# Optimization experiments

Measured on AMD Instinct MI355X. Metric: run time of the kernel, lower is better.

## Reference

```python
import jax, jax.numpy as jnp
import numpy as np

C = 128                  # stem_dim
CONV_DIM = C * C * 3 * 3 # 147456
B, T = 32, 30
N_CH = 1024
N_ANS = 32               # n_answers + 1
V = 44

UNARY = [4,10,11,12,13,14,15,16,17,18,19,20,21,22,23,24,25,29,30,31,32,33,34,35,36,37,38,39,40,41,43]
BINARY = [5,6,7,8,9,26,27,28,42]
SCENE_TOK = 4

_kind = np.zeros(V, np.int32)   # 0=special, 1=scene, 2=unary, 3=binary
_uidx = np.zeros(V, np.int32)
_bidx = np.zeros(V, np.int32)
for _j, _t in enumerate(UNARY):
    _kind[_t] = 2; _uidx[_t] = _j
for _j, _t in enumerate(BINARY):
    _kind[_t] = 3; _bidx[_t] = _j
_kind[SCENE_TOK] = 1
KIND_T, U_T, B_T = jnp.array(_kind), jnp.array(_uidx), jnp.array(_bidx)


def conv3x3(x, w):  # x [N,C,H,W], w [O,I,3,3], pad=1
    return jax.lax.conv_general_dilated(x, w, (1, 1), ((1, 1), (1, 1)),
                                        dimension_numbers=('NCHW', 'OIHW', 'NCHW'))


def conv1x1(x, w):
    return jax.lax.conv_general_dilated(x, w, (1, 1), ((0, 0), (0, 0)),
                                        dimension_numbers=('NCHW', 'OIHW', 'NCHW'))

# per-sample weights: vmap conv over batch
_bconv = jax.vmap(lambda x, w: conv3x3(x[None], w)[0])


def exec_unary(x, w1, w2):
    return jax.nn.relu(_bconv(jax.nn.relu(_bconv(x, w1)), w2))


def exec_binary(x1, x2, w1, w2, w3):
    h = jax.nn.relu(_bconv(jnp.concatenate([x1, x2], axis=1), w1))
    h = jax.nn.relu(_bconv(h, w2))
    return jax.nn.relu(_bconv(h, w3))


def setup_inputs() -> dict:
    key = jax.random.key(0)
    ks = jax.random.split(key, 10)
    std = 1.0 / float(np.sqrt(CONV_DIM))
    r = lambda k, shp, s: jax.random.normal(k, shp, jnp.float32) * s
    return {
        'feats': jax.random.normal(ks[0], (B, N_CH, 14, 14), jnp.float32),
        'programs': jax.random.randint(ks[1], (B, T), 0, V, dtype=jnp.int32),
        'stem_w1': r(ks[2], (C, N_CH, 3, 3), 0.02),
        'stem_b1': jnp.zeros((C,), jnp.float32),
        'stem_w2': r(ks[3], (C, C, 3, 3), 0.05),
        'stem_b2': jnp.zeros((C,), jnp.float32),
        'mem_u': jax.random.uniform(ks[4], (31, 2 * CONV_DIM), jnp.float32, -std, std),
        'mem_b': jax.random.uniform(ks[5], (9, 4 * CONV_DIM), jnp.float32, -std, std),
        'cls_w': r(ks[6], (512, C, 1, 1), 0.05),
        'cls_b': jnp.zeros((512,), jnp.float32),
        'fc1_w': r(ks[7], (1024, 512 * 7 * 7), 0.01),
        'fc1_b': jnp.zeros((1024,), jnp.float32),
        'fc2_w': r(ks[8], (N_ANS, 1024), 0.03),
        'fc2_b': jnp.zeros((N_ANS,), jnp.float32),
    }


def reference(feats, programs, stem_w1, stem_b1, stem_w2, stem_b2, mem_u, mem_b,
              cls_w, cls_b, fc1_w, fc1_b, fc2_w, fc2_b):
    # stem: conv3x3 -> relu -> conv3x3 -> relu
    h = jax.nn.relu(conv3x3(feats, stem_w1) + stem_b1[None, :, None, None])
    feat = jax.nn.relu(conv3x3(h, stem_w2) + stem_b2[None, :, None, None])  # [B,C,14,14]

    def step(carry, tok):  # tok [B] int32
        out, saved = carry
        kind = KIND_T[tok]                           # [B]
        uread = mem_u[U_T[tok]]                      # [B, 2*CONV_DIM] one-hot memory read
        w1 = uread[:, :CONV_DIM].reshape(-1, C, C, 3, 3)
        w2 = uread[:, CONV_DIM:].reshape(-1, C, C, 3, 3)
        bread = mem_b[B_T[tok]]                      # [B, 4*CONV_DIM]
        bw1 = bread[:, :2 * CONV_DIM].reshape(-1, C, 2 * C, 3, 3)
        bw2 = bread[:, 2 * CONV_DIM:3 * CONV_DIM].reshape(-1, C, C, 3, 3)
        bw3 = bread[:, 3 * CONV_DIM:].reshape(-1, C, C, 3, 3)
        is_scene = (kind == 1)[:, None, None, None]
        u_in = jnp.where(is_scene, feat, out)        # scene runs on stem features
        u_out = exec_unary(u_in, w1, w2)
        b_out = exec_binary(out, saved, bw1, bw2, bw3)
        k4 = kind[:, None, None, None]
        new_saved = jnp.where(is_scene, out, saved)  # scene saves current output
        new_out = jnp.where(k4 == 0, out, jnp.where(k4 == 3, b_out, u_out))
        return (new_out, new_saved), None

    toks_rev = programs[:, ::-1].T.astype(jnp.int32)  # [T,B] reversed program
    (out, _), _ = jax.lax.scan(step, (feat, jnp.zeros_like(feat)), toks_rev)

    # classifier: conv1x1 -> relu -> maxpool2 -> flatten -> fc -> relu -> fc
    h = jax.nn.relu(conv1x1(out, cls_w) + cls_b[None, :, None, None])
    h = jax.lax.reduce_window(h, -jnp.inf, jax.lax.max, (1, 1, 2, 2), (1, 1, 2, 2), 'VALID')
    h = h.reshape(h.shape[0], -1)                     # [B, 512*7*7]
    h = jax.nn.relu(h @ fc1_w.T + fc1_b)
    return h @ fc2_w.T + fc2_b                        # [B, N_ANS]
```

## Files before the change

kernel.cpp:

```cpp
#include <hip/hip_runtime.h>


#define NSTEP 30
#define CD 147456
#define P 196
#define FSZ 25088
#define LROW 18
#define LBUF (272*LROW)

typedef __attribute__((ext_vector_type(8))) short short8;
typedef __attribute__((ext_vector_type(16))) float f32x16;

__constant__ int KIND_TBL[44] = {
  0,0,0,0,1,3,3,3,3,3, 2,2,2,2,2,2,2,2,2,2,
  2,2,2,2,2,2,3,3,3,2, 2,2,2,2,2,2,2,2,2,2, 2,2,3,2};
__constant__ int MIDX_TBL[44] = {
  0,0,0,0,0,0,1,2,3,4, 1,2,3,4,5,6,7,8,9,10,
  11,12,13,14,15,16,5,6,7,17, 18,19,20,21,22,23,24,25,26,27, 28,29,8,30};

__device__ __forceinline__ uint32_t bf16_rne(float x) {
  uint32_t u = __float_as_uint(x);
  return (u + 0x7fffu + ((u >> 16) & 1u)) >> 16;
}
__device__ __forceinline__ uint32_t pack_hl(float x) {
  uint32_t h = bf16_rne(x);
  float rest = x - __uint_as_float(h << 16);
  uint32_t l = bf16_rne(rest);
  return (h << 16) | l;
}
__device__ __forceinline__ float ld_sc0(const float* p) {
  return __hip_atomic_load(p, __ATOMIC_RELAXED, __HIP_MEMORY_SCOPE_AGENT);
}

__device__ __forceinline__ void bbar(int* __restrict__ ctr, int target) {
  __syncthreads();
  if (threadIdx.x == 0) {
    __hip_atomic_fetch_add(ctr, 1, __ATOMIC_RELEASE, __HIP_MEMORY_SCOPE_AGENT);
    while (__hip_atomic_load(ctr, __ATOMIC_ACQUIRE, __HIP_MEMORY_SCOPE_AGENT) < target)
      __builtin_amdgcn_s_sleep(2);
  }
  __syncthreads();
}

__global__ void __launch_bounds__(256) repack_kernel(
    const float* __restrict__ sw1, const float* __restrict__ sw2,
    const float* __restrict__ mu, const float* __restrict__ mb,
    uint32_t* __restrict__ Wp)
{
  const int blk = blockIdx.x;
  const int C = blk / 9, tap = blk % 9;
  const float* src; int nic, lc;
  if (C < 64)       { src = sw1; nic = 1024; lc = C; }
  else if (C < 72)  { src = sw2; nic = 128;  lc = C - 64; }
  else if (C < 568) { int u = (C - 72) >> 4, r = (C - 72) & 15;
                      src = mu + (size_t)u * 2 * CD + (size_t)(r >> 3) * CD;
                      nic = 128; lc = r & 7; }
  else              { int j = (C - 568) >> 5, r = (C - 568) & 31;
                      const float* base = mb + (size_t)j * 4 * CD;
                      if (r < 16)      { src = base;                  nic = 256; lc = r; }
                      else if (r < 24) { src = base + 2 * (size_t)CD; nic = 128; lc = r - 16; }
                      else             { src = base + 3 * (size_t)CD; nic = 128; lc = r - 24; } }
  const int mt = threadIdx.x >> 6, lane = threadIdx.x & 63;
  const int oc = mt * 32 + (lane & 31);
  const int ic0 = lc * 16 + (lane >> 5) * 8;
  uint32_t hw[4], lw[4];
#pragma unroll
  for (int pr = 0; pr < 4; ++pr) {
    uint32_t hh[2], ll[2];
#pragma unroll
    for (int e = 0; e < 2; ++e) {
      float x = src[((size_t)oc * nic + (ic0 + pr * 2 + e)) * 9 + tap];
      uint32_t h = bf16_rne(x);
      float rest = x - __uint_as_float(h << 16);
      hh[e] = h; ll[e] = bf16_rne(rest);
    }
    hw[pr] = hh[0] | (hh[1] << 16);
    lw[pr] = ll[0] | (ll[1] << 16);
  }
  uint32_t* dstb = Wp + (size_t)blk * 2048;
  *(uint4*)(dstb + (mt * 2 + 0) * 256 + lane * 4) = make_uint4(hw[0], hw[1], hw[2], hw[3]);
  *(uint4*)(dstb + (mt * 2 + 1) * 256 + lane * 4) = make_uint4(lw[0], lw[1], lw[2], lw[3]);
}

union BU { uint32_t u[4]; uint4 v; short8 s8; };

__device__ __forceinline__ void load_wchunk(const uint32_t* __restrict__ wb,
                                            BU* wh, BU* wl) {
#pragma unroll
  for (int t = 0; t < 9; ++t) {
    wh[t].v = *(const uint4*)(wb + t * 2048);
    wl[t].v = *(const uint4*)(wb + t * 2048 + 256);
  }
}

__device__ __forceinline__ void mfma_chunk(const uint32_t* __restrict__ sb,
                                           int pwbase, const BU* wh, const BU* wl,
                                           f32x16& acc) {
  const int TAPOFF[9] = {0, 1, 2, 16, 17, 18, 32, 33, 34};
#pragma unroll
  for (int tap = 0; tap < 9; ++tap) {
    const int pw = pwbase + TAPOFF[tap] * LROW;
    uint2 q0 = *(const uint2*)(sb + pw);
    uint2 q1 = *(const uint2*)(sb + pw + 2);
    uint2 q2 = *(const uint2*)(sb + pw + 4);
    uint2 q3 = *(const uint2*)(sb + pw + 6);
    BU Bh, Bl;
    Bh.u[0] = __builtin_amdgcn_perm(q0.y, q0.x, 0x07060302u);
    Bh.u[1] = __builtin_amdgcn_perm(q1.y, q1.x, 0x07060302u);
    Bh.u[2] = __builtin_amdgcn_perm(q2.y, q2.x, 0x07060302u);
    Bh.u[3] = __builtin_amdgcn_perm(q3.y, q3.x, 0x07060302u);
    Bl.u[0] = __builtin_amdgcn_perm(q0.y, q0.x, 0x05040100u);
    Bl.u[1] = __builtin_amdgcn_perm(q1.y, q1.x, 0x05040100u);
    Bl.u[2] = __builtin_amdgcn_perm(q2.y, q2.x, 0x05040100u);
    Bl.u[3] = __builtin_amdgcn_perm(q3.y, q3.x, 0x05040100u);
    acc = __builtin_amdgcn_mfma_f32_32x32x16_bf16(wh[tap].s8, Bh.s8, acc, 0, 0, 0);
    acc = __builtin_amdgcn_mfma_f32_32x32x16_bf16(wh[tap].s8, Bl.s8, acc, 0, 0, 0);
    acc = __builtin_amdgcn_mfma_f32_32x32x16_bf16(wl[tap].s8, Bh.s8, acc, 0, 0, 0);
  }
}

__device__ __forceinline__ void conv_run(
    uint32_t sbuf[2][LBUF],
    const float* __restrict__ in0, const float* __restrict__ in1, int split, int nc,
    int C0, int mt,
    const uint32_t* __restrict__ Wp, const float* __restrict__ bias,
    float* __restrict__ dst, float* __restrict__ dst2, float* __restrict__ zb,
    const int* imgoff)
{
  const int tid = threadIdx.x;
  const int w = tid >> 6, lane = tid & 63, l31 = lane & 31, kq = lane >> 5;
  const int ic16 = tid >> 5, pl = tid & 31;
  const int pwbase = (32 * w + l31) * LROW + kq * 8;
  const bool cw = (w < 7);
  const uint32_t* wbase = Wp + (size_t)C0 * 9 * 2048 + (mt * 2) * 256 + lane * 4;

  f32x16 acc;
#pragma unroll
  for (int i = 0; i < 16; ++i) acc[i] = 0.f;

  BU whA[9], wlA[9], whB[9], wlB[9];
  if (cw) load_wchunk(wbase, whA, wlA);
  {
    const float* src = in0 + (size_t)ic16 * P;
#pragma unroll
    for (int i = 0; i < 9; ++i) {
      int p = pl + 32 * i;
      if (p < 272) {
        int off = imgoff[i];
        float x = (off >= 0) ? ld_sc0(src + off) : 0.f;
        sbuf[0][p * LROW + ic16] = pack_hl(x);
      }
    }
  }
  __syncthreads();

  int c = 0;
  while (true) {
    {
      const bool more = c + 1 < nc;
      float sv[9];
      if (more) {
        const int cn = c + 1;
        const float* src = (cn < split) ? in0 + (size_t)(cn * 16 + ic16) * P
                                        : in1 + (size_t)((cn - split) * 16 + ic16) * P;
#pragma unroll
        for (int i = 0; i < 9; ++i) {
          int off = imgoff[i];
          sv[i] = (off >= 0) ? ld_sc0(src + off) : 0.f;
        }
        if (cw) load_wchunk(wbase + (size_t)(c + 1) * 9 * 2048, whB, wlB);
      }
      if (cw) mfma_chunk(&sbuf[c & 1][0], pwbase, whA, wlA, acc);
      if (more) {
#pragma unroll
        for (int i = 0; i < 9; ++i) {
          int p = pl + 32 * i;
          if (p < 272) sbuf[(c + 1) & 1][p * LROW + ic16] = pack_hl(sv[i]);
        }
      }
      __syncthreads();
      if (++c >= nc) break;
    }
    {
      const bool more = c + 1 < nc;
      float sv[9];
      if (more) {
        const int cn = c + 1;
        const float* src = (cn < split) ? in0 + (size_t)(cn * 16 + ic16) * P
                                        : in1 + (size_t)((cn - split) * 16 + ic16) * P;
#pragma unroll
        for (int i = 0; i < 9; ++i) {
          int off = imgoff[i];
          sv[i] = (off >= 0) ? ld_sc0(src + off) : 0.f;
        }
        if (cw) load_wchunk(wbase + (size_t)(c + 1) * 9 * 2048, whA, wlA);
      }
      if (cw) mfma_chunk(&sbuf[c & 1][0], pwbase, whB, wlB, acc);
      if (more) {
#pragma unroll
        for (int i = 0; i < 9; ++i) {
          int p = pl + 32 * i;
          if (p < 272) sbuf[(c + 1) & 1][p * LROW + ic16] = pack_hl(sv[i]);
        }
      }
      __syncthreads();
      if (++c >= nc) break;
    }
  }

  if (cw) {
    const int ox = l31 & 15, oy = 2 * w + (l31 >> 4);
    if (ox < 14) {
#pragma unroll
      for (int reg = 0; reg < 16; ++reg) {
        int row = (reg & 3) + 8 * (reg >> 2) + 4 * kq;
        int oc = mt * 32 + row;
        float v = acc[reg];
        if (bias) v += bias[row];
        v = fmaxf(v, 0.f);
        dst[(size_t)oc * P + oy * 14 + ox] = v;
        if (dst2) dst2[(size_t)oc * P + oy * 14 + ox] = v;
        if (zb)   zb[(size_t)oc * P + oy * 14 + ox] = 0.f;
      }
    }
  }
}

__global__ void __launch_bounds__(512, 2) persist_kernel(
    const float* __restrict__ feats, const int* __restrict__ progs,
    const float* __restrict__ sb1, const float* __restrict__ sb2,
    const uint32_t* __restrict__ Wp,
    float* __restrict__ feat, float* __restrict__ outb, float* __restrict__ saved,
    float* __restrict__ h1, float* __restrict__ h2, int* __restrict__ ctr)
{
  __shared__ uint32_t s_act[2][LBUF];
  const int tid = threadIdx.x;
  const int b = blockIdx.x >> 2;
  const int mt = blockIdx.x & 3;
  const size_t bo = (size_t)b * FSZ;
  int* myctr = ctr + b * 32;
  int phase = 0;

  int imgoff[9];
#pragma unroll
  for (int i = 0; i < 9; ++i) {
    int p = (tid & 31) + 32 * i;
    int row = p >> 4, col = p & 15;
    imgoff[i] = (p < 272 && row >= 1 && row <= 14 && col >= 1 && col <= 14)
                ? (row - 1) * 14 + (col - 1) : -1;
  }

  conv_run(s_act, feats + (size_t)b * 1024 * P, nullptr, 1 << 28, 64, 0, mt, Wp,
           sb1 + mt * 32, h1 + bo, nullptr, nullptr, imgoff);
  bbar(myctr, ++phase * 4);
  conv_run(s_act, h1 + bo, nullptr, 1 << 28, 8, 64, mt, Wp,
           sb2 + mt * 32, feat + bo, outb + bo, saved + bo, imgoff);
  bbar(myctr, ++phase * 4);

  for (int s = 0; s < NSTEP; ++s) {
    int tok = progs[b * NSTEP + (NSTEP - 1 - s)];
    int kind = KIND_TBL[tok], mi = MIDX_TBL[tok];
    if (kind == 0) continue;
    if (kind == 1) {
      const size_t so = bo + (size_t)mt * 32 * P;
      for (int i = tid; i < 32 * P; i += 512)
        saved[so + i] = ld_sc0(&outb[so + i]);
      int C0 = 72 + mi * 16;
      conv_run(s_act, feat + bo, nullptr, 1 << 28, 8, C0, mt, Wp, nullptr,
               h1 + bo, nullptr, nullptr, imgoff);
      bbar(myctr, ++phase * 4);
      conv_run(s_act, h1 + bo, nullptr, 1 << 28, 8, C0 + 8, mt, Wp, nullptr,
               outb + bo, nullptr, nullptr, imgoff);
      bbar(myctr, ++phase * 4);
    } else if (kind == 2) {
      int C0 = 72 + mi * 16;
      conv_run(s_act, outb + bo, nullptr, 1 << 28, 8, C0, mt, Wp, nullptr,
               h1 + bo, nullptr, nullptr, imgoff);
      bbar(myctr, ++phase * 4);
      conv_run(s_act, h1 + bo, nullptr, 1 << 28, 8, C0 + 8, mt, Wp, nullptr,
               outb + bo, nullptr, nullptr, imgoff);
      bbar(myctr, ++phase * 4);
    } else {
      int C0 = 568 + mi * 32;
      conv_run(s_act, outb + bo, saved + bo, 8, 16, C0, mt, Wp, nullptr,
               h1 + bo, nullptr, nullptr, imgoff);
      bbar(myctr, ++phase * 4);
      conv_run(s_act, h1 + bo, nullptr, 1 << 28, 8, C0 + 16, mt, Wp, nullptr,
               h2 + bo, nullptr, nullptr, imgoff);
      bbar(myctr, ++phase * 4);
      conv_run(s_act, h2 + bo, nullptr, 1 << 28, 8, C0 + 24, mt, Wp, nullptr,
               outb + bo, nullptr, nullptr, imgoff);
      bbar(myctr, ++phase * 4);
    }
  }
}

__global__ void __launch_bounds__(256) cls_pool_kernel(
    const float* __restrict__ x, const float* __restrict__ Wc,
    const float* __restrict__ bc, float* __restrict__ hB)
{
  const int b = blockIdx.y, og = blockIdx.x;
  const int oc0 = og * 64;
  __shared__ float s[16 * P];
  const float* xb = x + (size_t)b * FSZ;
  const int tid = threadIdx.x;
  float acc[13][4];
#pragma unroll
  for (int k = 0; k < 13; ++k) { acc[k][0] = acc[k][1] = acc[k][2] = acc[k][3] = 0.f; }
  for (int c0 = 0; c0 < 128; c0 += 16) {
    __syncthreads();
    for (int i = tid; i < 16 * P; i += 256) s[i] = xb[(size_t)c0 * P + i];
    __syncthreads();
#pragma unroll
    for (int k = 0; k < 13; ++k) {
      const int idx = k * 256 + tid;
      if (idx < 64 * 49) {
        const int oc = oc0 + idx / 49, pp = idx % 49;
        const int py = pp / 7, px = pp % 7;
        const int b0 = 2 * py * 14 + 2 * px, b1 = b0 + 14;
        const float* wr = Wc + (size_t)oc * 128 + c0;
#pragma unroll
        for (int ic = 0; ic < 16; ++ic) {
          const float w = wr[ic];
          const float* sp = s + ic * P;
          const float2 r0 = *(const float2*)(sp + b0);
          const float2 r1 = *(const float2*)(sp + b1);
          acc[k][0] = fmaf(w, r0.x, acc[k][0]);
          acc[k][1] = fmaf(w, r0.y, acc[k][1]);
          acc[k][2] = fmaf(w, r1.x, acc[k][2]);
          acc[k][3] = fmaf(w, r1.y, acc[k][3]);
        }
      }
    }
  }
#pragma unroll
  for (int k = 0; k < 13; ++k) {
    const int idx = k * 256 + tid;
    if (idx < 64 * 49) {
      const int oc = oc0 + idx / 49, pp = idx % 49;
      const float m = fmaxf(fmaxf(acc[k][0], acc[k][1]), fmaxf(acc[k][2], acc[k][3]));
      hB[(size_t)b * 25088 + (size_t)oc * 49 + pp] = fmaxf(m + bc[oc], 0.f);
    }
  }
}

__global__ void __launch_bounds__(256) transpose_kernel(
    const float* __restrict__ hB, float* __restrict__ hT)
{
  __shared__ float t[256 * 33];
  const int k0 = blockIdx.x * 256;
  const int tid = threadIdx.x;
  for (int b = 0; b < 32; ++b)
    t[tid * 33 + b] = hB[(size_t)b * 25088 + k0 + tid];
  __syncthreads();
  for (int i = tid; i < 256 * 32; i += 256) {
    const int k = i >> 5, b = i & 31;
    hT[(size_t)(k0 + k) * 32 + b] = t[k * 33 + b];
  }
}

__global__ void __launch_bounds__(256) fc1_kernel(
    const float* __restrict__ hT, const float* __restrict__ W,
    const float* __restrict__ bias, float* __restrict__ o)
{
  const int b = threadIdx.x & 31, j = threadIdx.x >> 5;
  const int oc = blockIdx.x * 4 + (j & 3);
  const int kh = j >> 2;
  const float* wr = W + (size_t)oc * 25088 + (size_t)kh * 12544;
  const float* ht = hT + (size_t)kh * 12544 * 32;
  float acc = 0.f;
  for (int k = 0; k < 12544; k += 4) {
    const float4 w4 = *(const float4*)(wr + k);
    acc = fmaf(ht[(size_t)(k + 0) * 32 + b], w4.x, acc);
    acc = fmaf(ht[(size_t)(k + 1) * 32 + b], w4.y, acc);
    acc = fmaf(ht[(size_t)(k + 2) * 32 + b], w4.z, acc);
    acc = fmaf(ht[(size_t)(k + 3) * 32 + b], w4.w, acc);
  }
  __shared__ float red[8][32];
  red[j][b] = acc;
  __syncthreads();
  if (j < 4)
    o[(size_t)b * 1024 + oc] = fmaxf(red[j][b] + red[j + 4][b] + bias[oc], 0.f);
}

__global__ void __launch_bounds__(256) fc2_kernel(
    const float* __restrict__ h, const float* __restrict__ W,
    const float* __restrict__ bias, float* __restrict__ out)
{
  const int i = blockIdx.x * 256 + threadIdx.x;
  const int b = i >> 5, oo = i & 31;
  const float* wr = W + (size_t)oo * 1024;
  const float* hr = h + (size_t)b * 1024;
  float acc = bias[oo];
  for (int k = 0; k < 1024; k += 4) {
    const float4 w4 = *(const float4*)(wr + k);
    const float4 h4 = *(const float4*)(hr + k);
    acc = fmaf(h4.x, w4.x, acc);
    acc = fmaf(h4.y, w4.y, acc);
    acc = fmaf(h4.z, w4.z, acc);
    acc = fmaf(h4.w, w4.w, acc);
  }
  out[i] = acc;
}

extern "C" void kernel_launch(void* const* d_in, const int* in_sizes, int n_in,
                              void* d_out, int out_size, void* d_ws, size_t ws_size,
                              hipStream_t stream) {
  const float* feats   = (const float*)d_in[0];
  const int*   progs   = (const int*)  d_in[1];
  const float* stem_w1 = (const float*)d_in[2];
  const float* stem_b1 = (const float*)d_in[3];
  const float* stem_w2 = (const float*)d_in[4];
  const float* stem_b2 = (const float*)d_in[5];
  const float* mem_u   = (const float*)d_in[6];
  const float* mem_b   = (const float*)d_in[7];
  const float* cls_w   = (const float*)d_in[8];
  const float* cls_b   = (const float*)d_in[9];
  const float* fc1_w   = (const float*)d_in[10];
  const float* fc1_b   = (const float*)d_in[11];
  const float* fc2_w   = (const float*)d_in[12];
  const float* fc2_b   = (const float*)d_in[13];

  float* ws = (float*)d_ws;
  const size_t F = (size_t)32 * FSZ;
  float*    feat  = ws;
  float*    outb  = ws + 1 * F;
  float*    saved = ws + 2 * F;
  float*    h1    = ws + 3 * F;
  float*    h2    = ws + 4 * F;
  uint32_t* Wp    = (uint32_t*)(ws + 5 * F);
  int*      ctr   = (int*)(Wp + (size_t)7704 * 2048);

  hipMemsetAsync(ctr, 0, 32 * 32 * sizeof(int), stream);

  repack_kernel<<<dim3(7704), dim3(256), 0, stream>>>(stem_w1, stem_w2, mem_u, mem_b, Wp);

  persist_kernel<<<dim3(128), dim3(512), 0, stream>>>(
      feats, progs, stem_b1, stem_b2, Wp, feat, outb, saved, h1, h2, ctr);

  float* hB   = h1;
  float* hT   = h2;
  float* fc1o = saved;
  cls_pool_kernel<<<dim3(8, 32), dim3(256), 0, stream>>>(outb, cls_w, cls_b, hB);
  transpose_kernel<<<dim3(98), dim3(256), 0, stream>>>(hB, hT);
  fc1_kernel<<<dim3(256), dim3(256), 0, stream>>>(hT, fc1_w, fc1_b, fc1o);
  fc2_kernel<<<dim3(4), dim3(256), 0, stream>>>(fc1o, fc2_w, fc2_b, (float*)d_out);
}
```

Before: 3.350 ms.

## Split persistent conv blocks by image half and coalesce weight repack via LDS

The persistent kernel now runs 256 blocks of 256 threads, each handling half of the 14x14 image rows for one batch sample and output-channel tile. Each block stages a smaller padded activation tile in shared memory, and the per-sample barrier now waits for 8 blocks instead of 4. The aim is to put more CUs to work and use all waves for MFMA, where before one of eight waves sat idle. The weight repack kernel now loads contiguous weight slabs into LDS and transposes them there, so global reads are coalesced. The cost is redundant halo loads at the row split and twice the weight traffic per sample, since both halves load the same weights.

New measurement: 3.588 ms. +7.1%, slower.

```diff
diff --git a/kernel.cpp b/kernel.cpp
--- a/kernel.cpp
+++ b/kernel.cpp
@@ -6,7 +6,8 @@
 #define P 196
 #define FSZ 25088
 #define LROW 18
-#define LBUF (272*LROW)
+#define LPOS 176
+#define LBUF (LPOS*LROW)
 
 typedef __attribute__((ext_vector_type(8))) short short8;
 typedef __attribute__((ext_vector_type(16))) float f32x16;
@@ -47,8 +48,8 @@
     const float* __restrict__ mu, const float* __restrict__ mb,
     uint32_t* __restrict__ Wp)
 {
-  const int blk = blockIdx.x;
-  const int C = blk / 9, tap = blk % 9;
+  __shared__ float lds[64 * 144];
+  const int C = blockIdx.x;
   const float* src; int nic, lc;
   if (C < 64)       { src = sw1; nic = 1024; lc = C; }
   else if (C < 72)  { src = sw2; nic = 128;  lc = C - 64; }
@@ -60,26 +61,39 @@
                       if (r < 16)      { src = base;                  nic = 256; lc = r; }
                       else if (r < 24) { src = base + 2 * (size_t)CD; nic = 128; lc = r - 16; }
                       else             { src = base + 3 * (size_t)CD; nic = 128; lc = r - 24; } }
-  const int mt = threadIdx.x >> 6, lane = threadIdx.x & 63;
-  const int oc = mt * 32 + (lane & 31);
-  const int ic0 = lc * 16 + (lane >> 5) * 8;
-  uint32_t hw[4], lw[4];
-#pragma unroll
-  for (int pr = 0; pr < 4; ++pr) {
-    uint32_t hh[2], ll[2];
-#pragma unroll
-    for (int e = 0; e < 2; ++e) {
-      float x = src[((size_t)oc * nic + (ic0 + pr * 2 + e)) * 9 + tap];
-      uint32_t h = bf16_rne(x);
-      float rest = x - __uint_as_float(h << 16);
-      hh[e] = h; ll[e] = bf16_rne(rest);
-    }
-    hw[pr] = hh[0] | (hh[1] << 16);
-    lw[pr] = ll[0] | (ll[1] << 16);
-  }
-  uint32_t* dstb = Wp + (size_t)blk * 2048;
-  *(uint4*)(dstb + (mt * 2 + 0) * 256 + lane * 4) = make_uint4(hw[0], hw[1], hw[2], hw[3]);
-  *(uint4*)(dstb + (mt * 2 + 1) * 256 + lane * 4) = make_uint4(lw[0], lw[1], lw[2], lw[3]);
+  const int tid = threadIdx.x;
+  uint32_t* outc = Wp + (size_t)C * 9 * 2048;
+#pragma unroll
+  for (int pass = 0; pass < 2; ++pass) {
+    const int oc0 = pass * 64;
+    for (int k = 0; k < 36; ++k) {
+      int i = tid + 256 * k;
+      int ocl = i / 144, e = i - ocl * 144;
+      lds[i] = src[((size_t)(oc0 + ocl) * nic + lc * 16) * 9 + e];
+    }
+    __syncthreads();
+    for (int k = 0; k < 36; ++k) {
+      int o = tid + 256 * k;
+      int tap = o / 1024, r = o - tap * 1024;
+      int mtl = r >> 9, hl = (r >> 8) & 1, lane = (r >> 2) & 63, q = o & 3;
+      int ocl = mtl * 32 + (lane & 31);
+      int icl = (lane >> 5) * 8 + q * 2;
+      float x0 = lds[ocl * 144 + icl * 9 + tap];
+      float x1 = lds[ocl * 144 + (icl + 1) * 9 + tap];
+      uint32_t h0 = bf16_rne(x0), h1 = bf16_rne(x1);
+      uint32_t v;
+      if (hl) {
+        uint32_t l0 = bf16_rne(x0 - __uint_as_float(h0 << 16));
+        uint32_t l1 = bf16_rne(x1 - __uint_as_float(h1 << 16));
+        v = l0 | (l1 << 16);
+      } else {
+        v = h0 | (h1 << 16);
+      }
+      int mt = pass * 2 + mtl;
+      outc[tap * 2048 + mt * 512 + hl * 256 + lane * 4 + q] = v;
+    }
+    __syncthreads();
+  }
 }
 
 union BU { uint32_t u[4]; uint4 v; short8 s8; };
@@ -122,34 +136,30 @@
 __device__ __forceinline__ void conv_run(
     uint32_t sbuf[2][LBUF],
     const float* __restrict__ in0, const float* __restrict__ in1, int split, int nc,
-    int C0, int mt,
+    int C0, int mt, int half,
     const uint32_t* __restrict__ Wp, const float* __restrict__ bias,
     float* __restrict__ dst, float* __restrict__ dst2, float* __restrict__ zb,
     const int* imgoff)
 {
   const int tid = threadIdx.x;
   const int w = tid >> 6, lane = tid & 63, l31 = lane & 31, kq = lane >> 5;
-  const int ic16 = tid >> 5, pl = tid & 31;
+  const int ic16 = tid >> 4, pl = tid & 15;
   const int pwbase = (32 * w + l31) * LROW + kq * 8;
-  const bool cw = (w < 7);
-  const uint32_t* wbase = Wp + (size_t)C0 * 9 * 2048 + (mt * 2) * 256 + lane * 4;
+  const uint32_t* wbase = Wp + (size_t)C0 * 9 * 2048 + mt * 512 + lane * 4;
 
   f32x16 acc;
 #pragma unroll
   for (int i = 0; i < 16; ++i) acc[i] = 0.f;
 
   BU whA[9], wlA[9], whB[9], wlB[9];
-  if (cw) load_wchunk(wbase, whA, wlA);
+  load_wchunk(wbase, whA, wlA);
   {
     const float* src = in0 + (size_t)ic16 * P;
 #pragma unroll
     for (int i = 0; i < 9; ++i) {
-      int p = pl + 32 * i;
-      if (p < 272) {
-        int off = imgoff[i];
-        float x = (off >= 0) ? ld_sc0(src + off) : 0.f;
-        sbuf[0][p * LROW + ic16] = pack_hl(x);
-      }
+      int off = imgoff[i];
+      float x = (off >= 0) ? ld_sc0(src + off) : 0.f;
+      sbuf[0][(pl + 16 * i) * LROW + ic16] = pack_hl(x);
     }
   }
   __syncthreads();
@@ -168,15 +178,13 @@
           int off = imgoff[i];
           sv[i] = (off >= 0) ? ld_sc0(src + off) : 0.f;
         }
-        if (cw) load_wchunk(wbase + (size_t)(c + 1) * 9 * 2048, whB, wlB);
-      }
-      if (cw) mfma_chunk(&sbuf[c & 1][0], pwbase, whA, wlA, acc);
+        load_wchunk(wbase + (size_t)(c + 1) * 9 * 2048, whB, wlB);
+      }
+      mfma_chunk(&sbuf[c & 1][0], pwbase, whA, wlA, acc);
       if (more) {
 #pragma unroll
-        for (int i = 0; i < 9; ++i) {
-          int p = pl + 32 * i;
-          if (p < 272) sbuf[(c + 1) & 1][p * LROW + ic16] = pack_hl(sv[i]);
-        }
+        for (int i = 0; i < 9; ++i)
+          sbuf[(c + 1) & 1][(pl + 16 * i) * LROW + ic16] = pack_hl(sv[i]);
       }
       __syncthreads();
       if (++c >= nc) break;
@@ -193,24 +201,23 @@
           int off = imgoff[i];
           sv[i] = (off >= 0) ? ld_sc0(src + off) : 0.f;
         }
-        if (cw) load_wchunk(wbase + (size_t)(c + 1) * 9 * 2048, whA, wlA);
-      }
-      if (cw) mfma_chunk(&sbuf[c & 1][0], pwbase, whB, wlB, acc);
+        load_wchunk(wbase + (size_t)(c + 1) * 9 * 2048, whA, wlA);
+      }
+      mfma_chunk(&sbuf[c & 1][0], pwbase, whB, wlB, acc);
       if (more) {
 #pragma unroll
-        for (int i = 0; i < 9; ++i) {
-          int p = pl + 32 * i;
-          if (p < 272) sbuf[(c + 1) & 1][p * LROW + ic16] = pack_hl(sv[i]);
-        }
+        for (int i = 0; i < 9; ++i)
+          sbuf[(c + 1) & 1][(pl + 16 * i) * LROW + ic16] = pack_hl(sv[i]);
       }
       __syncthreads();
       if (++c >= nc) break;
     }
   }
 
-  if (cw) {
-    const int ox = l31 & 15, oy = 2 * w + (l31 >> 4);
-    if (ox < 14) {
+  {
+    const int ox = l31 & 15, oyl = 2 * w + (l31 >> 4);
+    if (ox < 14 && oyl < 7) {
+      const int oy = half * 7 + oyl;
 #pragma unroll
       for (int reg = 0; reg < 16; ++reg) {
         int row = (reg & 3) + 8 * (reg >> 2) + 4 * kq;
@@ -226,7 +233,7 @@
   }
 }
 
-__global__ void __launch_bounds__(512, 2) persist_kernel(
+__global__ void __launch_bounds__(256, 2) persist_kernel(
     const float* __restrict__ feats, const int* __restrict__ progs,
     const float* __restrict__ sb1, const float* __restrict__ sb2,
     const uint32_t* __restrict__ Wp,
@@ -235,62 +242,68 @@
 {
   __shared__ uint32_t s_act[2][LBUF];
   const int tid = threadIdx.x;
-  const int b = blockIdx.x >> 2;
-  const int mt = blockIdx.x & 3;
+  const int idx = blockIdx.x;
+  const int half = idx >> 7;
+  const int bm = idx & 127;
+  const int b = bm >> 2, mt = bm & 3;
   const size_t bo = (size_t)b * FSZ;
   int* myctr = ctr + b * 32;
   int phase = 0;
 
   int imgoff[9];
-#pragma unroll
-  for (int i = 0; i < 9; ++i) {
-    int p = (tid & 31) + 32 * i;
-    int row = p >> 4, col = p & 15;
-    imgoff[i] = (p < 272 && row >= 1 && row <= 14 && col >= 1 && col <= 14)
-                ? (row - 1) * 14 + (col - 1) : -1;
-  }
-
-  conv_run(s_act, feats + (size_t)b * 1024 * P, nullptr, 1 << 28, 64, 0, mt, Wp,
+  {
+    const int pl = tid & 15;
+    const int gc = pl - 1;
+#pragma unroll
+    for (int i = 0; i < 9; ++i) {
+      int gr = half * 7 + i - 1;
+      imgoff[i] = (gr >= 0 && gr < 14 && gc >= 0 && gc < 14) ? gr * 14 + gc : -1;
+    }
+  }
+
+  conv_run(s_act, feats + (size_t)b * 1024 * P, nullptr, 1 << 28, 64, 0, mt, half, Wp,
            sb1 + mt * 32, h1 + bo, nullptr, nullptr, imgoff);
-  bbar(myctr, ++phase * 4);
-  conv_run(s_act, h1 + bo, nullptr, 1 << 28, 8, 64, mt, Wp,
+  bbar(myctr, ++phase * 8);
+  conv_run(s_act, h1 + bo, nullptr, 1 << 28, 8, 64, mt, half, Wp,
            sb2 + mt * 32, feat + bo, outb + bo, saved + bo, imgoff);
-  bbar(myctr, ++phase * 4);
+  bbar(myctr, ++phase * 8);
 
   for (int s = 0; s < NSTEP; ++s) {
     int tok = progs[b * NSTEP + (NSTEP - 1 - s)];
     int kind = KIND_TBL[tok], mi = MIDX_TBL[tok];
     if (kind == 0) continue;
     if (kind == 1) {
-      const size_t so = bo + (size_t)mt * 32 * P;
-      for (int i = tid; i < 32 * P; i += 512)
-        saved[so + i] = ld_sc0(&outb[so + i]);
+      for (int i = tid; i < 32 * 98; i += 256) {
+        int ch = i / 98, pos = i - ch * 98 + half * 98;
+        size_t a = bo + (size_t)(mt * 32 + ch) * P + pos;
+        saved[a] = ld_sc0(&outb[a]);
+      }
       int C0 = 72 + mi * 16;
-      conv_run(s_act, feat + bo, nullptr, 1 << 28, 8, C0, mt, Wp, nullptr,
+      conv_run(s_act, feat + bo, nullptr, 1 << 28, 8, C0, mt, half, Wp, nullptr,
                h1 + bo, nullptr, nullptr, imgoff);
-      bbar(myctr, ++phase * 4);
-      conv_run(s_act, h1 + bo, nullptr, 1 << 28, 8, C0 + 8, mt, Wp, nullptr,
+      bbar(myctr, ++phase * 8);
+      conv_run(s_act, h1 + bo, nullptr, 1 << 28, 8, C0 + 8, mt, half, Wp, nullptr,
                outb + bo, nullptr, nullptr, imgoff);
-      bbar(myctr, ++phase * 4);
+      bbar(myctr, ++phase * 8);
     } else if (kind == 2) {
       int C0 = 72 + mi * 16;
-      conv_run(s_act, outb + bo, nullptr, 1 << 28, 8, C0, mt, Wp, nullptr,
+      conv_run(s_act, outb + bo, nullptr, 1 << 28, 8, C0, mt, half, Wp, nullptr,
                h1 + bo, nullptr, nullptr, imgoff);
-      bbar(myctr, ++phase * 4);
-      conv_run(s_act, h1 + bo, nullptr, 1 << 28, 8, C0 + 8, mt, Wp, nullptr,
+      bbar(myctr, ++phase * 8);
+      conv_run(s_act, h1 + bo, nullptr, 1 << 28, 8, C0 + 8, mt, half, Wp, nullptr,
                outb + bo, nullptr, nullptr, imgoff);
-      bbar(myctr, ++phase * 4);
+      bbar(myctr, ++phase * 8);
     } else {
       int C0 = 568 + mi * 32;
-      conv_run(s_act, outb + bo, saved + bo, 8, 16, C0, mt, Wp, nullptr,
+      conv_run(s_act, outb + bo, saved + bo, 8, 16, C0, mt, half, Wp, nullptr,
                h1 + bo, nullptr, nullptr, imgoff);
-      bbar(myctr, ++phase * 4);
-      conv_run(s_act, h1 + bo, nullptr, 1 << 28, 8, C0 + 16, mt, Wp, nullptr,
+      bbar(myctr, ++phase * 8);
+      conv_run(s_act, h1 + bo, nullptr, 1 << 28, 8, C0 + 16, mt, half, Wp, nullptr,
                h2 + bo, nullptr, nullptr, imgoff);
-      bbar(myctr, ++phase * 4);
-      conv_run(s_act, h2 + bo, nullptr, 1 << 28, 8, C0 + 24, mt, Wp, nullptr,
+      bbar(myctr, ++phase * 8);
+      conv_run(s_act, h2 + bo, nullptr, 1 << 28, 8, C0 + 24, mt, half, Wp, nullptr,
                outb + bo, nullptr, nullptr, imgoff);
-      bbar(myctr, ++phase * 4);
+      bbar(myctr, ++phase * 8);
     }
   }
 }
@@ -429,13 +442,13 @@
   float*    h1    = ws + 3 * F;
   float*    h2    = ws + 4 * F;
   uint32_t* Wp    = (uint32_t*)(ws + 5 * F);
-  int*      ctr   = (int*)(Wp + (size_t)7704 * 2048);
+  int*      ctr   = (int*)(Wp + (size_t)856 * 9 * 2048);
 
   hipMemsetAsync(ctr, 0, 32 * 32 * sizeof(int), stream);
 
-  repack_kernel<<<dim3(7704), dim3(256), 0, stream>>>(stem_w1, stem_w2, mem_u, mem_b, Wp);
-
-  persist_kernel<<<dim3(128), dim3(512), 0, stream>>>(
+  repack_kernel<<<dim3(856), dim3(256), 0, stream>>>(stem_w1, stem_w2, mem_u, mem_b, Wp);
+
+  persist_kernel<<<dim3(256), dim3(256), 0, stream>>>(
       feats, progs, stem_b1, stem_b2, Wp, feat, outb, saved, h1, h2, ctr);
 
   float* hB   = h1;
```
